# Kernel optimization log

Measured on AMD Instinct MI355X. Metric: run time of the kernel, lower is better.

## Reference

```python
import jax, jax.numpy as jnp
import numpy as np


def setup_inputs() -> dict:
    key = jax.random.key(0)
    ks = jax.random.split(key, 12)
    B, IN, H = 4096, 512, 1024
    s = lambda k, shape, scale: jax.random.normal(k, shape, dtype=jnp.float32) * scale
    inp = {
        "inputs": s(ks[0], (B, IN), 1.0),
        "h0": s(ks[1], (B, H), 1.0),
        "c0": s(ks[2], (B, H), 1.0),
        "ts": jax.random.uniform(ks[3], (B, 2), dtype=jnp.float32),
        "w_ih": s(ks[4], (4 * H, IN), 1.0 / np.sqrt(IN)),
        "w_hh": s(ks[5], (4 * H, H), 1.0 / np.sqrt(H)),
        "b_ih": s(ks[6], (4 * H,), 1.0 / np.sqrt(H)),
        "b_hh": s(ks[7], (4 * H,), 1.0 / np.sqrt(H)),
        "w1": s(ks[8], (H, H), 1.0 / np.sqrt(H)),
        "b1": s(ks[9], (H,), 1.0 / np.sqrt(H)),
        "w2": s(ks[10], (H, H), 1.0 / np.sqrt(H)),
        "b2": s(ks[11], (H,), 1.0 / np.sqrt(H)),
    }
    return inp


def _lstm_cell(x, h, c, w_ih, w_hh, b_ih, b_hh):
    # gates: [B, 4H] in PyTorch (i, f, g, o) order
    gates = x @ w_ih.T + h @ w_hh.T + b_ih + b_hh
    i, f, g, o = jnp.split(gates, 4, axis=-1)
    i, f, o = jax.nn.sigmoid(i), jax.nn.sigmoid(f), jax.nn.sigmoid(o)
    g = jnp.tanh(g)
    c_new = f * c + i * g
    h_new = o * jnp.tanh(c_new)
    return h_new, c_new


def reference(inputs, h0, c0, ts, w_ih, w_hh, b_ih, b_hh, w1, b1, w2, b2):
    # Two stacked LSTMCell applications sharing the same weights
    h, c = _lstm_cell(inputs, h0, c0, w_ih, w_hh, b_ih, b_hh)
    h, c = _lstm_cell(inputs, h, c, w_ih, w_hh, b_ih, b_hh)

    # Autonomous ODE func: Linear -> Tanh -> Linear
    f = lambda y: jnp.tanh(y @ w1.T + b1) @ w2.T + b2

    # One RK4 step per sample from ts[:,0] to ts[:,1] (batched, no python loop)
    dt = (ts[:, 1] - ts[:, 0])[:, None]  # [B, 1]
    k1 = f(h)
    k2 = f(h + 0.5 * dt * k1)
    k3 = f(h + 0.5 * dt * k2)
    k4 = f(h + dt * k3)
    ht = h + (dt / 6.0) * (k1 + 2.0 * k2 + 2.0 * k3 + k4)
    return (ht, c)
```

## Files before the change

### kernel.cpp

```cpp
#include <hip/hip_runtime.h>

typedef short short8 __attribute__((ext_vector_type(8)));
typedef float f32x4 __attribute__((ext_vector_type(4)));
typedef unsigned short u16x8 __attribute__((ext_vector_type(8)));

#define B_DIM 4096
#define IN_DIM 512
#define H_DIM 1024
#define KCAT 1536

__device__ __forceinline__ float bs2f(unsigned short s) {
    return __uint_as_float(((unsigned int)s) << 16);
}
__device__ __forceinline__ unsigned short f2bs(float f) {
    unsigned int u = __float_as_uint(f);
    u += 0x7fff + ((u >> 16) & 1);
    return (unsigned short)(u >> 16);
}
__device__ __forceinline__ float sigm(float x) { return 1.0f / (1.0f + __expf(-x)); }
__device__ __forceinline__ float ftanh(float x) { return 1.0f - 2.0f / (__expf(2.0f * x) + 1.0f); }

__device__ __forceinline__ int gperm(int r) {
    int g = r >> 10, j = r & 1023;
    return ((j >> 4) << 6) + (g << 4) + (j & 15);
}

#define T0 262144
#define T1 786432
#define T2 1048576
#define T3 1572864
#define T4 1703936
#define T5 1835008
__device__ __forceinline__ u16x8 cvt8(const float* __restrict__ in, long i) {
    float4 a = *(const float4*)(in + i);
    float4 b = *(const float4*)(in + i + 4);
    u16x8 o;
    o[0] = f2bs(a.x); o[1] = f2bs(a.y); o[2] = f2bs(a.z); o[3] = f2bs(a.w);
    o[4] = f2bs(b.x); o[5] = f2bs(b.y); o[6] = f2bs(b.z); o[7] = f2bs(b.w);
    return o;
}
__global__ __launch_bounds__(256) void pack_all(const float* __restrict__ x,
                                                const float* __restrict__ h0,
                                                const float* __restrict__ wih,
                                                const float* __restrict__ whh,
                                                const float* __restrict__ w1,
                                                const float* __restrict__ w2,
                                                unsigned short* __restrict__ xb,
                                                unsigned short* __restrict__ hb0,
                                                unsigned short* __restrict__ wcat,
                                                unsigned short* __restrict__ w116,
                                                unsigned short* __restrict__ w216) {
    long g = (long)blockIdx.x * 256 + threadIdx.x;
    if (g < T0) {
        long i = g * 8;
        *(u16x8*)(xb + i) = cvt8(x, i);
    } else if (g < T1) {
        long i = (g - T0) * 8;
        *(u16x8*)(hb0 + i) = cvt8(h0, i);
    } else if (g < T2) {
        long i = (g - T1) * 8;
        int r = (int)(i / IN_DIM), c = (int)(i % IN_DIM);
        *(u16x8*)(wcat + (size_t)gperm(r) * KCAT + c) = cvt8(wih, i);
    } else if (g < T3) {
        long i = (g - T2) * 8;
        int r = (int)(i / H_DIM), c = (int)(i % H_DIM);
        *(u16x8*)(wcat + (size_t)gperm(r) * KCAT + IN_DIM + c) = cvt8(whh, i);
    } else if (g < T4) {
        long i = (g - T3) * 8;
        *(u16x8*)(w116 + i) = cvt8(w1, i);
    } else if (g < T5) {
        long i = (g - T4) * 8;
        *(u16x8*)(w216 + i) = cvt8(w2, i);
    }
}

__global__ __launch_bounds__(256) void prep_small(const float* __restrict__ bih,
                                                  const float* __restrict__ bhh,
                                                  const float* __restrict__ ts,
                                                  float* __restrict__ bsum,
                                                  float* __restrict__ dtv,
                                                  int n4h, int nb) {
    int i = blockIdx.x * blockDim.x + threadIdx.x;
    if (i < n4h) bsum[gperm(i)] = bih[i] + bhh[i];
    if (i < nb)  dtv[i] = ts[2 * i + 1] - ts[2 * i];
}

#define NT8 (KCAT / 32)

__global__ __launch_bounds__(512) void gemm8(
    const unsigned short* __restrict__ xb,
    const unsigned short* __restrict__ hb,
    const unsigned short* __restrict__ W,
    const float* __restrict__ bias,
    unsigned short* __restrict__ h_out,
    float* __restrict__ c_out,
    const float* __restrict__ c_in) {
    __shared__ unsigned short lA[4][256 * 32];
    __shared__ unsigned short lB[4][256 * 32];
    const int t = threadIdx.x;
    const int lane = t & 63;
    const int wave = t >> 6;
    const int wm = (wave >> 2) * 128;
    const int wn = (wave & 3) * 64;
    const int fr = lane & 15;
    const int kb = lane >> 4;
    const int tile_m = blockIdx.y * 256;
    const int tile_n = blockIdx.x * 256;

    f32x4 acc[8][4];
    #pragma unroll
    for (int i = 0; i < 8; ++i)
        #pragma unroll
        for (int j = 0; j < 4; ++j)
            acc[i][j] = (f32x4){0.f, 0.f, 0.f, 0.f};

    auto stageA = [&](int kt) {
        const int buf = kt & 3;
        #pragma unroll
        for (int j = 0; j < 2; ++j) {
            int idx = j * 512 + t;
            int row = idx >> 2;
            int g = idx & 3;
            int gs = g ^ ((row >> 1) & 3);
            int kk = kt * 32 + gs * 8;
            const unsigned short* src = (kk < IN_DIM)
                ? xb + (size_t)(tile_m + row) * IN_DIM + kk
                : hb + (size_t)(tile_m + row) * H_DIM + (kk - IN_DIM);
            __builtin_amdgcn_global_load_lds(
                (__attribute__((address_space(1))) void*)src,
                (__attribute__((address_space(3))) void*)(&lA[buf][row * 32 + g * 8]), 16, 0, 0);
        }
    };
    auto stageB = [&](int kt) {
        const int buf = kt & 3;
        #pragma unroll
        for (int j = 0; j < 2; ++j) {
            int idx = j * 512 + t;
            int row = idx >> 2;
            int g = idx & 3;
            int gs = g ^ ((row >> 1) & 3);
            int kk = kt * 32 + gs * 8;
            __builtin_amdgcn_global_load_lds(
                (__attribute__((address_space(1))) void*)(W + (size_t)(tile_n + row) * KCAT + kk),
                (__attribute__((address_space(3))) void*)(&lB[buf][row * 32 + g * 8]), 16, 0, 0);
        }
    };

    stageA(0); stageB(0);
    stageA(1); stageB(1);
    stageA(2); stageB(2);
    asm volatile("s_waitcnt vmcnt(8)" ::: "memory");
    __builtin_amdgcn_s_barrier();

    for (int kt = 0; kt < NT8; ++kt) {
        const int buf = kt & 3;
        short8 bfr[4], af[4];
        #pragma unroll
        for (int j = 0; j < 4; ++j) {
            int brow = wn + j * 16 + fr;
            bfr[j] = *(const short8*)&lB[buf][brow * 32 + (kb ^ ((brow >> 1) & 3)) * 8];
        }
        #pragma unroll
        for (int i = 0; i < 4; ++i) {
            int arow = wm + i * 16 + fr;
            af[i] = *(const short8*)&lA[buf][arow * 32 + (kb ^ ((arow >> 1) & 3)) * 8];
        }
        if (kt + 3 < NT8) stageA(kt + 3);
        __builtin_amdgcn_s_barrier();
        __builtin_amdgcn_s_setprio(1);
        #pragma unroll
        for (int i = 0; i < 4; ++i)
            #pragma unroll
            for (int j = 0; j < 4; ++j)
                acc[i][j] = __builtin_amdgcn_mfma_f32_16x16x32_bf16(af[i], bfr[j], acc[i][j], 0, 0, 0);
        __builtin_amdgcn_s_setprio(0);
        asm volatile("" ::: "memory");
        __builtin_amdgcn_s_barrier();
        short8 af2[4];
        #pragma unroll
        for (int i = 0; i < 4; ++i) {
            int arow = wm + 64 + i * 16 + fr;
            af2[i] = *(const short8*)&lA[buf][arow * 32 + (kb ^ ((arow >> 1) & 3)) * 8];
        }
        if (kt + 3 < NT8) stageB(kt + 3);
        if (kt + 3 < NT8)      asm volatile("s_waitcnt vmcnt(8)" ::: "memory");
        else if (kt + 2 < NT8) asm volatile("s_waitcnt vmcnt(4)" ::: "memory");
        else if (kt + 1 < NT8) asm volatile("s_waitcnt vmcnt(0)" ::: "memory");
        __builtin_amdgcn_s_barrier();
        __builtin_amdgcn_s_setprio(1);
        #pragma unroll
        for (int i = 0; i < 4; ++i)
            #pragma unroll
            for (int j = 0; j < 4; ++j)
                acc[4 + i][j] = __builtin_amdgcn_mfma_f32_16x16x32_bf16(af2[i], bfr[j], acc[4 + i][j], 0, 0, 0);
        __builtin_amdgcn_s_setprio(0);
        asm volatile("" ::: "memory");
        __builtin_amdgcn_s_barrier();
    }

    const int jbase = ((tile_n + wn) >> 6) << 4;
    float bv[4];
    #pragma unroll
    for (int g = 0; g < 4; ++g) bv[g] = bias[tile_n + wn + g * 16 + fr];
    #pragma unroll
    for (int i = 0; i < 8; ++i) {
        #pragma unroll
        for (int r = 0; r < 4; ++r) {
            const int m = tile_m + wm + i * 16 + kb * 4 + r;
            const int j = jbase + fr;
            float ig = sigm(acc[i][0][r] + bv[0]);
            float fg = sigm(acc[i][1][r] + bv[1]);
            float gg = ftanh(acc[i][2][r] + bv[2]);
            float og = sigm(acc[i][3][r] + bv[3]);
            float cin = c_in[(size_t)m * H_DIM + j];
            float cn = fg * cin + ig * gg;
            float hn = og * ftanh(cn);
            h_out[(size_t)m * H_DIM + j] = f2bs(hn);
            c_out[(size_t)m * H_DIM + j] = cn;
        }
    }
}

#define BKt 32

template <int EPI, int BM, int BN>
__global__ __launch_bounds__(256) void gemm2(
    const unsigned short* __restrict__ A1,
    const unsigned short* __restrict__ W,
    const int M, const int N, const int K,
    const float* __restrict__ bias,
    unsigned short* __restrict__ outb,
    float* __restrict__ outf,
    const unsigned short* __restrict__ hmat,
    const float* __restrict__ dtv,
    float* __restrict__ S,
    unsigned short* __restrict__ ynext,
    const float alpha, const float cw, const int first) {
    constexpr int WM = BM / 2;
    constexpr int WN = BN / 2;
    constexpr int MR = WM / 16;
    constexpr int NR = WN / 16;
    constexpr int ALOADS = BM * BKt / 8 / 256;
    constexpr int BLOADS = BN * BKt / 8 / 256;
    constexpr int LIF = ALOADS + BLOADS;

    __shared__ unsigned short lA[2][BM * BKt];
    __shared__ unsigned short lB[2][BN * BKt];
    const int t = threadIdx.x;
    const int lane = t & 63;
    const int wave = t >> 6;
    const int wm = (wave >> 1) * WM;
    const int wn = (wave & 1) * WN;
    const int fr = lane & 15;
    const int kb = lane >> 4;
    const int tile_m = blockIdx.y * BM;
    const int tile_n = blockIdx.x * BN;

    f32x4 acc[MR][NR];
    #pragma unroll
    for (int i = 0; i < MR; ++i)
        #pragma unroll
        for (int j = 0; j < NR; ++j)
            acc[i][j] = (f32x4){0.f, 0.f, 0.f, 0.f};

    const unsigned short* aptr1 = A1 + (size_t)tile_m * K;
    const unsigned short* wptr  = W + (size_t)tile_n * K;

    auto stage = [&](int buf, int k0) {
        #pragma unroll
        for (int j = 0; j < ALOADS; ++j) {
            int idx = j * 256 + t;
            int row = idx >> 2;
            int col = ((idx & 3) ^ ((row >> 1) & 3)) * 8;
            __builtin_amdgcn_global_load_lds(
                (__attribute__((address_space(1))) void*)(aptr1 + (size_t)row * K + k0 + col),
                (__attribute__((address_space(3))) void*)(&lA[buf][idx * 8]), 16, 0, 0);
        }
        #pragma unroll
        for (int j = 0; j < BLOADS; ++j) {
            int idx = j * 256 + t;
            int row = idx >> 2;
            int col = ((idx & 3) ^ ((row >> 1) & 3)) * 8;
            __builtin_amdgcn_global_load_lds(
                (__attribute__((address_space(1))) void*)(wptr + (size_t)row * K + k0 + col),
                (__attribute__((address_space(3))) void*)(&lB[buf][idx * 8]), 16, 0, 0);
        }
    };

    const int NT = K / BKt;
    stage(0, 0);
    if (NT > 1) stage(1, BKt);
    int cur = 0;
    for (int kt = 0; kt < NT; ++kt) {
        if (kt + 1 < NT) {
            if constexpr (LIF == 2) asm volatile("s_waitcnt vmcnt(2)" ::: "memory");
            else if constexpr (LIF == 3) asm volatile("s_waitcnt vmcnt(3)" ::: "memory");
            else if constexpr (LIF == 4) asm volatile("s_waitcnt vmcnt(4)" ::: "memory");
            else asm volatile("s_waitcnt vmcnt(0)" ::: "memory");
        } else {
            asm volatile("s_waitcnt vmcnt(0)" ::: "memory");
        }
        __builtin_amdgcn_s_barrier();
        short8 af[MR], bfr[NR];
        #pragma unroll
        for (int i = 0; i < MR; ++i) {
            const int arow = wm + i * 16 + fr;
            af[i] = *(const short8*)&lA[cur][arow * BKt + (kb ^ ((arow >> 1) & 3)) * 8];
        }
        #pragma unroll
        for (int j = 0; j < NR; ++j) {
            const int brow = wn + j * 16 + fr;
            bfr[j] = *(const short8*)&lB[cur][brow * BKt + (kb ^ ((brow >> 1) & 3)) * 8];
        }
        #pragma unroll
        for (int i = 0; i < MR; ++i)
            #pragma unroll
            for (int j = 0; j < NR; ++j)
                acc[i][j] = __builtin_amdgcn_mfma_f32_16x16x32_bf16(af[i], bfr[j], acc[i][j], 0, 0, 0);
        asm volatile("" ::: "memory");
        __builtin_amdgcn_s_barrier();
        if (kt + 2 < NT) stage(cur, (kt + 2) * BKt);
        cur ^= 1;
    }

    #pragma unroll
    for (int i = 0; i < MR; ++i) {
        #pragma unroll
        for (int r = 0; r < 4; ++r) {
            const int m = tile_m + wm + i * 16 + kb * 4 + r;
            float dt = 0.f;
            if (EPI >= 2) dt = dtv[m];
            #pragma unroll
            for (int j = 0; j < NR; ++j) {
                const int n = tile_n + wn + j * 16 + fr;
                const size_t off = (size_t)m * N + n;
                float v = acc[i][j][r];
                if (bias) v += bias[n];
                if (EPI == 1) {
                    outb[off] = f2bs(ftanh(v));
                } else if (EPI == 2) {
                    float hv = bs2f(hmat[off]);
                    float s = first ? 0.f : S[off];
                    S[off] = s + cw * v;
                    ynext[off] = f2bs(hv + alpha * dt * v);
                } else {
                    float hv = bs2f(hmat[off]);
                    outf[off] = hv + (dt * (1.0f / 6.0f)) * (S[off] + v);
                }
            }
        }
    }
}

extern "C" void kernel_launch(void* const* d_in, const int* in_sizes, int n_in,
                              void* d_out, int out_size, void* d_ws, size_t ws_size,
                              hipStream_t stream) {
    int IX = 0, IH0 = 1, IC0 = 2, ITS = 3, IWIH = 4, IWHH = 5, IBIH = 6, IBHH = 7,
        IW1 = 8, IB1 = 9, IW2 = 10, IB2 = 11;
    const bool sorted_ok = n_in >= 12 &&
        in_sizes[0] == 1024 && in_sizes[1] == 1024 && in_sizes[2] == 4096 &&
        in_sizes[3] == 4096 && in_sizes[4] == 4194304 && in_sizes[5] == 4194304 &&
        in_sizes[6] == 2097152 && in_sizes[7] == 8192 && in_sizes[8] == 1048576 &&
        in_sizes[9] == 1048576 && in_sizes[10] == 4194304 && in_sizes[11] == 2097152;
    if (sorted_ok) {
        IB1 = 0; IB2 = 1; IBHH = 2; IBIH = 3; IC0 = 4; IH0 = 5;
        IX = 6; ITS = 7; IW1 = 8; IW2 = 9; IWHH = 10; IWIH = 11;
    }
    const float* x_f   = (const float*)d_in[IX];
    const float* h0_f  = (const float*)d_in[IH0];
    const float* c0_f  = (const float*)d_in[IC0];
    const float* ts_f  = (const float*)d_in[ITS];
    const float* wih_f = (const float*)d_in[IWIH];
    const float* whh_f = (const float*)d_in[IWHH];
    const float* bih_f = (const float*)d_in[IBIH];
    const float* bhh_f = (const float*)d_in[IBHH];
    const float* w1_f  = (const float*)d_in[IW1];
    const float* b1_f  = (const float*)d_in[IB1];
    const float* w2_f  = (const float*)d_in[IW2];
    const float* b2_f  = (const float*)d_in[IB2];

    constexpr size_t SZ_BIN  = (size_t)B_DIM * IN_DIM;
    constexpr size_t SZ_BH   = (size_t)B_DIM * H_DIM;
    constexpr size_t SZ_HH   = (size_t)H_DIM * H_DIM;
    constexpr size_t SZ_WCAT = (size_t)4 * H_DIM * KCAT;

    float* bsum = (float*)d_ws;
    float* dtv  = bsum + 4 * H_DIM;
    float* S    = dtv + B_DIM;
    float* c1f  = S + SZ_BH;
    unsigned short* wcat = (unsigned short*)(c1f + SZ_BH);
    unsigned short* w116 = wcat + SZ_WCAT;
    unsigned short* w216 = w116 + SZ_HH;
    unsigned short* xb   = w216 + SZ_HH;
    unsigned short* hb0  = xb + SZ_BIN;
    unsigned short* hb1  = hb0 + SZ_BH;
    unsigned short* hb2  = hb1 + SZ_BH;
    unsigned short* ubuf = hb2 + SZ_BH;
    unsigned short* ybuf = ubuf + SZ_BH;

    float* out_ht = (float*)d_out;
    float* out_c  = out_ht + SZ_BH;

    const int TB = 256;
    pack_all<<<T5 / TB, TB, 0, stream>>>(x_f, h0_f, wih_f, whh_f, w1_f, w2_f,
                                         xb, hb0, wcat, w116, w216);
    prep_small<<<(4 * H_DIM) / TB, TB, 0, stream>>>(bih_f, bhh_f, ts_f, bsum, dtv, 4 * H_DIM, B_DIM);

    dim3 g8(4 * H_DIM / 256, B_DIM / 256);
    dim3 gSm(H_DIM / 64, B_DIM / 64);

    gemm8<<<g8, 512, 0, stream>>>(xb, hb0, wcat, bsum, hb1, c1f, c0_f);
    gemm8<<<g8, 512, 0, stream>>>(xb, hb1, wcat, bsum, hb2, out_c, c1f);

    gemm2<1, 64, 64><<<gSm, TB, 0, stream>>>(
        hb2, w116, B_DIM, H_DIM, H_DIM, b1_f,
        ubuf, nullptr, nullptr, nullptr, nullptr, nullptr, 0.f, 0.f, 0);
    gemm2<2, 64, 64><<<gSm, TB, 0, stream>>>(
        ubuf, w216, B_DIM, H_DIM, H_DIM, b2_f,
        nullptr, nullptr, hb2, dtv, S, ybuf, 0.5f, 1.0f, 1);
    gemm2<1, 64, 64><<<gSm, TB, 0, stream>>>(
        ybuf, w116, B_DIM, H_DIM, H_DIM, b1_f,
        ubuf, nullptr, nullptr, nullptr, nullptr, nullptr, 0.f, 0.f, 0);
    gemm2<2, 64, 64><<<gSm, TB, 0, stream>>>(
        ubuf, w216, B_DIM, H_DIM, H_DIM, b2_f,
        nullptr, nullptr, hb2, dtv, S, ybuf, 0.5f, 2.0f, 0);
    gemm2<1, 64, 64><<<gSm, TB, 0, stream>>>(
        ybuf, w116, B_DIM, H_DIM, H_DIM, b1_f,
        ubuf, nullptr, nullptr, nullptr, nullptr, nullptr, 0.f, 0.f, 0);
    gemm2<2, 64, 64><<<gSm, TB, 0, stream>>>(
        ubuf, w216, B_DIM, H_DIM, H_DIM, b2_f,
        nullptr, nullptr, hb2, dtv, S, ybuf, 1.0f, 2.0f, 0);
    gemm2<1, 64, 64><<<gSm, TB, 0, stream>>>(
        ybuf, w116, B_DIM, H_DIM, H_DIM, b1_f,
        ubuf, nullptr, nullptr, nullptr, nullptr, nullptr, 0.f, 0.f, 0);
    gemm2<3, 64, 64><<<gSm, TB, 0, stream>>>(
        ubuf, w216, B_DIM, H_DIM, H_DIM, b2_f,
        nullptr, out_ht, hb2, dtv, S, nullptr, 0.f, 0.f, 0);
}
```

Measured before the change: 338.5 us.

## Use 3-stage LDS ring buffers with one barrier per k-step in both GEMMs

The LSTM GEMM moves from a 4-buffer, two-half, four-barrier-per-iteration schedule to a 3-buffer ring that prefetches two tiles ahead. It loads all 8 A fragments at once and uses a single wait+barrier per k-tile. The RK4 GEMM goes from double to triple buffering, so its trailing barrier can be dropped and the next stage issued right after the MFMAs. This cuts barrier overhead and sync stalls, but gives up one stage of prefetch depth in the LSTM GEMM and raises register pressure from holding 8 A fragments.

```diff
diff --git a/kernel.cpp b/kernel.cpp
--- a/kernel.cpp
+++ b/kernel.cpp
@@ -95,8 +95,8 @@
     unsigned short* __restrict__ h_out,
     float* __restrict__ c_out,
     const float* __restrict__ c_in) {
-    __shared__ unsigned short lA[4][256 * 32];
-    __shared__ unsigned short lB[4][256 * 32];
+    __shared__ unsigned short lA[3][256 * 32];
+    __shared__ unsigned short lB[3][256 * 32];
     const int t = threadIdx.x;
     const int lane = t & 63;
     const int wave = t >> 6;
@@ -115,7 +115,7 @@
             acc[i][j] = (f32x4){0.f, 0.f, 0.f, 0.f};
 
     auto stageA = [&](int kt) {
-        const int buf = kt & 3;
+        const int buf = kt % 3;
         #pragma unroll
         for (int j = 0; j < 2; ++j) {
             int idx = j * 512 + t;
@@ -132,7 +132,7 @@
         }
     };
     auto stageB = [&](int kt) {
-        const int buf = kt & 3;
+        const int buf = kt % 3;
         #pragma unroll
         for (int j = 0; j < 2; ++j) {
             int idx = j * 512 + t;
@@ -148,54 +148,33 @@
 
     stageA(0); stageB(0);
     stageA(1); stageB(1);
-    stageA(2); stageB(2);
-    asm volatile("s_waitcnt vmcnt(8)" ::: "memory");
-    __builtin_amdgcn_s_barrier();
 
     for (int kt = 0; kt < NT8; ++kt) {
-        const int buf = kt & 3;
-        short8 bfr[4], af[4];
+        const int buf = kt % 3;
+        if (kt + 1 < NT8) asm volatile("s_waitcnt vmcnt(4)" ::: "memory");
+        else              asm volatile("s_waitcnt vmcnt(0)" ::: "memory");
+        __builtin_amdgcn_s_barrier();
+        asm volatile("" ::: "memory");
+        short8 bfr[4], af[8];
         #pragma unroll
         for (int j = 0; j < 4; ++j) {
             int brow = wn + j * 16 + fr;
             bfr[j] = *(const short8*)&lB[buf][brow * 32 + (kb ^ ((brow >> 1) & 3)) * 8];
         }
         #pragma unroll
-        for (int i = 0; i < 4; ++i) {
+        for (int i = 0; i < 8; ++i) {
             int arow = wm + i * 16 + fr;
             af[i] = *(const short8*)&lA[buf][arow * 32 + (kb ^ ((arow >> 1) & 3)) * 8];
         }
-        if (kt + 3 < NT8) stageA(kt + 3);
-        __builtin_amdgcn_s_barrier();
         __builtin_amdgcn_s_setprio(1);
         #pragma unroll
-        for (int i = 0; i < 4; ++i)
+        for (int i = 0; i < 8; ++i)
             #pragma unroll
             for (int j = 0; j < 4; ++j)
                 acc[i][j] = __builtin_amdgcn_mfma_f32_16x16x32_bf16(af[i], bfr[j], acc[i][j], 0, 0, 0);
         __builtin_amdgcn_s_setprio(0);
+        if (kt + 2 < NT8) { stageA(kt + 2); stageB(kt + 2); }
         asm volatile("" ::: "memory");
-        __builtin_amdgcn_s_barrier();
-        short8 af2[4];
-        #pragma unroll
-        for (int i = 0; i < 4; ++i) {
-            int arow = wm + 64 + i * 16 + fr;
-            af2[i] = *(const short8*)&lA[buf][arow * 32 + (kb ^ ((arow >> 1) & 3)) * 8];
-        }
-        if (kt + 3 < NT8) stageB(kt + 3);
-        if (kt + 3 < NT8)      asm volatile("s_waitcnt vmcnt(8)" ::: "memory");
-        else if (kt + 2 < NT8) asm volatile("s_waitcnt vmcnt(4)" ::: "memory");
-        else if (kt + 1 < NT8) asm volatile("s_waitcnt vmcnt(0)" ::: "memory");
-        __builtin_amdgcn_s_barrier();
-        __builtin_amdgcn_s_setprio(1);
-        #pragma unroll
-        for (int i = 0; i < 4; ++i)
-            #pragma unroll
-            for (int j = 0; j < 4; ++j)
-                acc[4 + i][j] = __builtin_amdgcn_mfma_f32_16x16x32_bf16(af2[i], bfr[j], acc[4 + i][j], 0, 0, 0);
-        __builtin_amdgcn_s_setprio(0);
-        asm volatile("" ::: "memory");
-        __builtin_amdgcn_s_barrier();
     }
 
     const int jbase = ((tile_n + wn) >> 6) << 4;
@@ -244,8 +223,8 @@
     constexpr int BLOADS = BN * BKt / 8 / 256;
     constexpr int LIF = ALOADS + BLOADS;
 
-    __shared__ unsigned short lA[2][BM * BKt];
-    __shared__ unsigned short lB[2][BN * BKt];
+    __shared__ unsigned short lA[3][BM * BKt];
+    __shared__ unsigned short lB[3][BN * BKt];
     const int t = threadIdx.x;
     const int lane = t & 63;
     const int wave = t >> 6;
@@ -266,7 +245,9 @@
     const unsigned short* aptr1 = A1 + (size_t)tile_m * K;
     const unsigned short* wptr  = W + (size_t)tile_n * K;
 
-    auto stage = [&](int buf, int k0) {
+    auto stage = [&](int kt) {
+        const int buf = kt % 3;
+        const int k0 = kt * BKt;
         #pragma unroll
         for (int j = 0; j < ALOADS; ++j) {
             int idx = j * 256 + t;
@@ -288,10 +269,10 @@
     };
 
     const int NT = K / BKt;
-    stage(0, 0);
-    if (NT > 1) stage(1, BKt);
-    int cur = 0;
+    stage(0);
+    if (NT > 1) stage(1);
     for (int kt = 0; kt < NT; ++kt) {
+        const int buf = kt % 3;
         if (kt + 1 < NT) {
             if constexpr (LIF == 2) asm volatile("s_waitcnt vmcnt(2)" ::: "memory");
             else if constexpr (LIF == 3) asm volatile("s_waitcnt vmcnt(3)" ::: "memory");
@@ -301,26 +282,25 @@
             asm volatile("s_waitcnt vmcnt(0)" ::: "memory");
         }
         __builtin_amdgcn_s_barrier();
+        asm volatile("" ::: "memory");
         short8 af[MR], bfr[NR];
         #pragma unroll
         for (int i = 0; i < MR; ++i) {
             const int arow = wm + i * 16 + fr;
-            af[i] = *(const short8*)&lA[cur][arow * BKt + (kb ^ ((arow >> 1) & 3)) * 8];
+            af[i] = *(const short8*)&lA[buf][arow * BKt + (kb ^ ((arow >> 1) & 3)) * 8];
         }
         #pragma unroll
         for (int j = 0; j < NR; ++j) {
             const int brow = wn + j * 16 + fr;
-            bfr[j] = *(const short8*)&lB[cur][brow * BKt + (kb ^ ((brow >> 1) & 3)) * 8];
+            bfr[j] = *(const short8*)&lB[buf][brow * BKt + (kb ^ ((brow >> 1) & 3)) * 8];
         }
         #pragma unroll
         for (int i = 0; i < MR; ++i)
             #pragma unroll
             for (int j = 0; j < NR; ++j)
                 acc[i][j] = __builtin_amdgcn_mfma_f32_16x16x32_bf16(af[i], bfr[j], acc[i][j], 0, 0, 0);
+        if (kt + 2 < NT) stage(kt + 2);
         asm volatile("" ::: "memory");
-        __builtin_amdgcn_s_barrier();
-        if (kt + 2 < NT) stage(cur, (kt + 2) * BKt);
-        cur ^= 1;
     }
 
     #pragma unroll
```

After: 338.8 us. No clear change (+0.1%).
